# Optimization experiments

Hardware: AMD Instinct MI355X
Metric: run time of the kernel (lower is better)

## Reference

```python
import jax, jax.numpy as jnp
import numpy as np

# ---- static problem configuration (matches init_kwargs) ----
N_PAIRS = 256
NODES_PER_GRAPH = 64
EDGES_PER_GRAPH = 200
MAX_EDGES = 256            # max_edge_set_size
N_GRAPHS = 2 * N_PAIRS     # query/corpus interleaved
N_NODES = N_GRAPHS * NODES_PER_GRAPH
N_EDGES = N_GRAPHS * EDGES_PER_GRAPH
NODE_DIM = 16
EDGE_DIM = 16
H = 128                    # node_state_dim
E_ENC = 64                 # encoded edge feature dim
MSG = 256                  # edge_hidden_sizes[-1] = 2*H (GMN GRU convention)
SK = 32                    # sinkhorn_feature_dim
PROP_STEPS = 5
SK_ITERS = 20
TEMP = 0.1


def setup_inputs() -> dict:
    key = jax.random.key(0)
    ks = jax.random.split(key, 16)
    node_features = jax.random.normal(ks[0], (N_NODES, NODE_DIM), jnp.float32)
    edge_features = jax.random.normal(ks[1], (N_EDGES, EDGE_DIM), jnp.float32)
    # edges are grouped per graph (graph g owns edges [g*E, (g+1)*E)) and
    # endpoints stay inside graph g's node range, as get_graph_features assumes
    offs = np.repeat(np.arange(N_GRAPHS) * NODES_PER_GRAPH, EDGES_PER_GRAPH)
    rng = np.random.default_rng(0)
    from_idx = jnp.asarray(offs + rng.integers(0, NODES_PER_GRAPH, N_EDGES), jnp.int32)
    to_idx = jnp.asarray(offs + rng.integers(0, NODES_PER_GRAPH, N_EDGES), jnp.int32)

    def lin(k, i, o):
        return jax.random.normal(k, (i, o), jnp.float32) / np.sqrt(i).astype(np.float32)

    p = dict(
        enc_node_w=lin(ks[2], NODE_DIM, H), enc_node_b=jnp.zeros((H,), jnp.float32),
        enc_edge_w=lin(ks[3], EDGE_DIM, E_ENC), enc_edge_b=jnp.zeros((E_ENC,), jnp.float32),
        msg_w1=lin(ks[4], 2 * H + E_ENC, MSG), msg_b1=jnp.zeros((MSG,), jnp.float32),
        msg_w2=lin(ks[5], MSG, MSG), msg_b2=jnp.zeros((MSG,), jnp.float32),
        rmsg_w1=lin(ks[6], 2 * H + E_ENC, MSG), rmsg_b1=jnp.zeros((MSG,), jnp.float32),
        rmsg_w2=lin(ks[7], MSG, MSG), rmsg_b2=jnp.zeros((MSG,), jnp.float32),
        gru_w_ih=lin(ks[8], MSG, 3 * H), gru_b_ih=jnp.zeros((3 * H,), jnp.float32),
        gru_w_hh=lin(ks[9], H, 3 * H), gru_b_hh=jnp.zeros((3 * H,), jnp.float32),
        sk_w1=lin(ks[10], MSG, SK), sk_b1=jnp.zeros((SK,), jnp.float32),
        sk_w2=lin(ks[11], SK, SK), sk_b2=jnp.zeros((SK,), jnp.float32),
    )
    return {"node_features": node_features, "edge_features": edge_features,
            "from_idx": from_idx, "to_idx": to_idx, **p}


def _mlp2(x, w1, b1, w2, b2):
    # Linear -> ReLU -> Linear (GMN MLP: no activation after last layer)
    return jax.nn.relu(x @ w1 + b1) @ w2 + b2


def reference(node_features, edge_features, from_idx, to_idx,
              enc_node_w, enc_node_b, enc_edge_w, enc_edge_b,
              msg_w1, msg_b1, msg_w2, msg_b2,
              rmsg_w1, rmsg_b1, rmsg_w2, rmsg_b2,
              gru_w_ih, gru_b_ih, gru_w_hh, gru_b_hh,
              sk_w1, sk_b1, sk_w2, sk_b2):
    # ---- GraphEncoder (single-layer MLPs) ----
    h = node_features @ enc_node_w + enc_node_b          # [N_NODES, H]
    e = edge_features @ enc_edge_w + enc_edge_b          # [N_EDGES, E_ENC]

    def edge_msgs(h):
        s, d = h[from_idx], h[to_idx]                    # gathers [N_EDGES, H]
        fwd = _mlp2(jnp.concatenate([s, d, e], axis=1), msg_w1, msg_b1, msg_w2, msg_b2)
        rev = _mlp2(jnp.concatenate([d, s, e], axis=1), rmsg_w1, rmsg_b1, rmsg_w2, rmsg_b2)
        return fwd, rev                                  # [N_EDGES, MSG] each

    # ---- propagation loop: gather -> edge MLP -> scatter -> GRU update ----
    for _ in range(PROP_STEPS):
        fwd, rev = edge_msgs(h)
        agg = (jax.ops.segment_sum(fwd, to_idx, num_segments=N_NODES)
               + jax.ops.segment_sum(rev, from_idx, num_segments=N_NODES))  # [N_NODES, MSG]
        gi = agg @ gru_w_ih + gru_b_ih                   # [N_NODES, 3H]
        gh = h @ gru_w_hh + gru_b_hh
        r = jax.nn.sigmoid(gi[:, :H] + gh[:, :H])
        z = jax.nn.sigmoid(gi[:, H:2 * H] + gh[:, H:2 * H])
        n = jnp.tanh(gi[:, 2 * H:] + r * gh[:, 2 * H:])
        h = (1.0 - z) * n + z * h                        # torch GRU update

    # ---- propagation_messages: per-edge fwd + rev message ----
    fwd, rev = edge_msgs(h)
    e_final = fwd + rev                                  # [N_EDGES, MSG]

    # ---- split_and_stack: per-graph edge sets padded to MAX_EDGES ----
    stacked = jnp.pad(e_final.reshape(N_GRAPHS, EDGES_PER_GRAPH, MSG),
                      ((0, 0), (0, MAX_EDGES - EDGES_PER_GRAPH), (0, 0)))
    q, c = stacked[0::2], stacked[1::2]                  # [B, MAX_EDGES, MSG]

    # ---- sinkhorn feature MLP + size mask ----
    tq = _mlp2(q, sk_w1, sk_b1, sk_w2, sk_b2)            # [B, MAX_EDGES, SK]
    tc = _mlp2(c, sk_w1, sk_b1, sk_w2, sk_b2)
    mask = (jnp.arange(MAX_EDGES) < EDGES_PER_GRAPH).astype(jnp.float32)[None, :, None]
    mq, mc = mask * tq, mask * tc

    # ---- log-domain Sinkhorn ----
    la = jnp.einsum('bif,bjf->bij', mq, mc) / TEMP       # [B, MAX_EDGES, MAX_EDGES]
    for _ in range(SK_ITERS):
        la = la - jax.nn.logsumexp(la, axis=2, keepdims=True)
        la = la - jax.nn.logsumexp(la, axis=1, keepdims=True)
    plan = jnp.exp(la)

    # ---- feature_alignment_score: -sum relu(q - P @ c) ----
    return -jnp.sum(jax.nn.relu(q - jnp.einsum('bij,bjf->bif', plan, c)), axis=(1, 2))
```

## Files before the change

### kernel.cpp

```cpp
#include <hip/hip_runtime.h>
#include <math.h>

typedef __attribute__((ext_vector_type(4))) float f32x4;
typedef __attribute__((ext_vector_type(8))) short s16x8;
typedef __attribute__((ext_vector_type(4))) short s16x4;

#define NN 32768
#define NE 102400
#define HD 128
#define EED 64
#define MSGD 256
#define NG 512
#define EPG 200
#define NP 256
#define SKD 32

__device__ inline short f2bf(float x){
  union{float f; unsigned u;} z; z.f=x;
  unsigned r = (z.u + 0x7fffu + ((z.u>>16)&1u)) >> 16;
  return (short)r;
}
__device__ inline float bf2f(unsigned short u){
  union{unsigned u; float f;} z; z.u = ((unsigned)u)<<16; return z.f;
}
__device__ inline float frcp(float x){
  float r; asm("v_rcp_f32 %0, %1" : "=v"(r) : "v"(x)); return r;
}

__global__ void __launch_bounds__(256) k_enc_node(const float* __restrict__ nf,
    const float* __restrict__ W, const float* __restrict__ b, float* __restrict__ h){
  __shared__ float Ws[16*128];
  int t = threadIdx.x;
  for (int i=t;i<16*128;i+=256) Ws[i]=W[i];
  __syncthreads();
  int node = blockIdx.x*2 + (t>>7);
  int f = t & 127;
  const float* x = nf + node*16;
  float acc = b[f];
  #pragma unroll
  for (int k=0;k<16;k++) acc = fmaf(x[k], Ws[k*128+f], acc);
  h[node*HD+f] = acc;
}

__global__ void __launch_bounds__(256) k_enc_edge(const float* __restrict__ ef,
    const float* __restrict__ W, const float* __restrict__ b, float* __restrict__ ee){
  __shared__ float Ws[16*64];
  int t = threadIdx.x;
  for (int i=t;i<16*64;i+=256) Ws[i]=W[i];
  __syncthreads();
  int edge = blockIdx.x*4 + (t>>6);
  int f = t & 63;
  const float* x = ef + edge*16;
  float acc = b[f];
  #pragma unroll
  for (int k=0;k<16;k++) acc = fmaf(x[k], Ws[k*64+f], acc);
  ee[edge*EED+f] = acc;
}

__global__ void __launch_bounds__(256) k_pack(const float* __restrict__ W,
    short* __restrict__ dst, int K, int N){
  int NT = N >> 4;
  int i = blockIdx.x*256 + threadIdx.x;
  if (i >= (K/32)*NT*64) return;
  int l = i & 63, tile = i >> 6;
  int nt = tile % NT, kt = tile / NT;
  int lr = l & 15, lq = l >> 4;
  s16x8 v;
  #pragma unroll
  for (int j=0;j<8;j++)
    v[j] = f2bf(W[(size_t)(kt*32 + lq*8 + j)*N + nt*16 + lr]);
  *((s16x8*)dst + i) = v;
}

__global__ void __launch_bounds__(256) k_csr_count(const int* __restrict__ fidx,
    const int* __restrict__ tidx, int* __restrict__ cur_in, int* __restrict__ cur_out){
  int e = blockIdx.x*256 + threadIdx.x;
  if (e >= NE) return;
  atomicAdd(&cur_in[tidx[e]], 1);
  atomicAdd(&cur_out[fidx[e]], 1);
}
__global__ void k_csr_scan(int* __restrict__ cur_in, int* __restrict__ start_in,
    int* __restrict__ cur_out, int* __restrict__ start_out){
  if (threadIdx.x) return;
  int g = blockIdx.x;
  int n0 = g*64, base = g*EPG;
  int run = base;
  for (int i=0;i<64;i++){ int c=cur_in[n0+i]; start_in[n0+i]=run; cur_in[n0+i]=run; run+=c; }
  run = base;
  for (int i=0;i<64;i++){ int c=cur_out[n0+i]; start_out[n0+i]=run; cur_out[n0+i]=run; run+=c; }
}
__global__ void __launch_bounds__(256) k_csr_fill(const int* __restrict__ fidx,
    const int* __restrict__ tidx, int* __restrict__ cur_in, int* __restrict__ cur_out,
    int* __restrict__ list_in, int* __restrict__ list_out){
  int e = blockIdx.x*256 + threadIdx.x;
  if (e >= NE) return;
  int p1 = atomicAdd(&cur_in[tidx[e]], 1);  list_in[p1] = e;
  int p2 = atomicAdd(&cur_out[fidx[e]], 1); list_out[p2] = e;
}

__global__ void __launch_bounds__(256,2) k_msg_both(const float* __restrict__ h,
    const float* __restrict__ ee, const int* __restrict__ from_idx, const int* __restrict__ to_idx,
    const short* __restrict__ w1f, const float* __restrict__ b1f,
    const short* __restrict__ w2f, const float* __restrict__ b2f,
    const short* __restrict__ w1r, const float* __restrict__ b1r,
    const short* __restrict__ w2r, const float* __restrict__ b2r,
    short* __restrict__ mf, short* __restrict__ mr){
  __shared__ __align__(16) short Xs[64][328];
  __shared__ __align__(16) short Ys[64][264];
  __shared__ int sidx[64], didx[64];
  int t = threadIdx.x;
  int e0 = blockIdx.x*64;
  if (t < 64){ sidx[t]=from_idx[e0+t]; didx[t]=to_idx[e0+t]; }
  __syncthreads();
  for (int i=t; i<64*40; i+=256){
    int r = i/40, c8 = (i - r*40)*8;
    const float* src; int off;
    if (c8 < 128){ src = h + (size_t)sidx[r]*HD; off = c8; }
    else if (c8 < 256){ src = h + (size_t)didx[r]*HD; off = c8-128; }
    else { src = ee + (size_t)(e0+r)*EED; off = c8-256; }
    float4 a = *(const float4*)(src+off);
    float4 b = *(const float4*)(src+off+4);
    s16x8 v;
    v[0]=f2bf(a.x); v[1]=f2bf(a.y); v[2]=f2bf(a.z); v[3]=f2bf(a.w);
    v[4]=f2bf(b.x); v[5]=f2bf(b.y); v[6]=f2bf(b.z); v[7]=f2bf(b.w);
    *(s16x8*)&Xs[r][c8] = v;
  }
  __syncthreads();

  int wv = t>>6, l = t&63, lr = l&15, lq = l>>4;
  int cbase = wv*64;

  for (int dir=0; dir<2; dir++){
    const s16x8* W1v = (const s16x8*)(dir ? w1r : w1f);
    const float* B1  = dir ? b1r : b1f;
    const s16x8* W2v = (const s16x8*)(dir ? w2r : w2f);
    const float* B2  = dir ? b2r : b2f;

    f32x4 acc[4][4];
    #pragma unroll
    for (int ct=0; ct<4; ct++){
      float bb = B1[cbase + ct*16 + lr];
      #pragma unroll
      for (int rt=0; rt<4; rt++) acc[rt][ct] = (f32x4){bb,bb,bb,bb};
    }
    {
      s16x8 a0[4], b0[4], b1[4];
      int sc0 = dir ? 4 : 0;
      #pragma unroll
      for (int rt=0;rt<4;rt++) a0[rt] = *(const s16x8*)&Xs[rt*16+lr][sc0*32 + lq*8];
      #pragma unroll
      for (int ct=0;ct<4;ct++) b0[ct] = W1v[(size_t)(0*16 + wv*4 + ct)*64 + l];
      #pragma unroll
      for (int ct=0;ct<4;ct++) b1[ct] = W1v[(size_t)(1*16 + wv*4 + ct)*64 + l];
      #pragma unroll
      for (int kt=0; kt<10; kt++){
        s16x8 an[4], bn[4];
        if (kt < 9){
          int sc = (dir && (kt+1)<8) ? ((kt+1)^4) : (kt+1);
          #pragma unroll
          for (int rt=0;rt<4;rt++) an[rt] = *(const s16x8*)&Xs[rt*16+lr][sc*32 + lq*8];
        }
        if (kt < 8){
          #pragma unroll
          for (int ct=0;ct<4;ct++) bn[ct] = W1v[(size_t)((kt+2)*16 + wv*4 + ct)*64 + l];
        }
        #pragma unroll
        for (int rt=0; rt<4; rt++)
          #pragma unroll
          for (int ct=0; ct<4; ct++)
            acc[rt][ct] = __builtin_amdgcn_mfma_f32_16x16x32_bf16(a0[rt], b0[ct], acc[rt][ct], 0,0,0);
        #pragma unroll
        for (int i=0;i<4;i++){ a0[i]=an[i]; b0[i]=b1[i]; b1[i]=bn[i]; }
      }
    }
    #pragma unroll
    for (int rt=0; rt<4; rt++)
      #pragma unroll
      for (int ct=0; ct<4; ct++)
        #pragma unroll
        for (int r=0; r<4; r++)
          Ys[rt*16 + lq*4 + r][cbase + ct*16 + lr] = f2bf(fmaxf(acc[rt][ct][r], 0.f));
    __syncthreads();

    f32x4 acc2[4][4];
    #pragma unroll
    for (int ct=0; ct<4; ct++){
      float bb = B2[cbase + ct*16 + lr];
      #pragma unroll
      for (int rt=0; rt<4; rt++) acc2[rt][ct] = (f32x4){bb,bb,bb,bb};
    }
    {
      s16x8 a0[4], b0[4], b1[4];
      #pragma unroll
      for (int rt=0;rt<4;rt++) a0[rt] = *(const s16x8*)&Ys[rt*16+lr][lq*8];
      #pragma unroll
      for (int ct=0;ct<4;ct++) b0[ct] = W2v[(size_t)(0*16 + wv*4 + ct)*64 + l];
      #pragma unroll
      for (int ct=0;ct<4;ct++) b1[ct] = W2v[(size_t)(1*16 + wv*4 + ct)*64 + l];
      #pragma unroll
      for (int kt=0; kt<8; kt++){
        s16x8 an[4], bn[4];
        if (kt < 7){
          #pragma unroll
          for (int rt=0;rt<4;rt++) an[rt] = *(const s16x8*)&Ys[rt*16+lr][(kt+1)*32 + lq*8];
        }
        if (kt < 6){
          #pragma unroll
          for (int ct=0;ct<4;ct++) bn[ct] = W2v[(size_t)((kt+2)*16 + wv*4 + ct)*64 + l];
        }
        #pragma unroll
        for (int rt=0; rt<4; rt++)
          #pragma unroll
          for (int ct=0; ct<4; ct++)
            acc2[rt][ct] = __builtin_amdgcn_mfma_f32_16x16x32_bf16(a0[rt], b0[ct], acc2[rt][ct], 0,0,0);
        #pragma unroll
        for (int i=0;i<4;i++){ a0[i]=an[i]; b0[i]=b1[i]; b1[i]=bn[i]; }
      }
    }
    __syncthreads();
    #pragma unroll
    for (int rt=0; rt<4; rt++)
      #pragma unroll
      for (int ct=0; ct<4; ct++)
        #pragma unroll
        for (int r=0; r<4; r++)
          Ys[rt*16 + lq*4 + r][cbase + ct*16 + lr] = f2bf(acc2[rt][ct][r]);
    __syncthreads();
    {
      short* dst = (dir ? mr : mf) + (size_t)e0*MSGD;
      for (int i=t; i<64*32; i+=256){
        int row = i>>5, c8 = (i&31)*8;
        *(s16x8*)&dst[(size_t)row*MSGD + c8] = *(const s16x8*)&Ys[row][c8];
      }
    }
    __syncthreads();
  }
}

__global__ void __launch_bounds__(256) k_gather(const unsigned short* __restrict__ mf,
    const unsigned short* __restrict__ mr,
    const int* __restrict__ start_in, const int* __restrict__ end_in, const int* __restrict__ list_in,
    const int* __restrict__ start_out, const int* __restrict__ end_out, const int* __restrict__ list_out,
    float* __restrict__ agg){
  int n = blockIdx.x*4 + (threadIdx.x>>6);
  int l = threadIdx.x & 63;
  float4 acc = {0.f,0.f,0.f,0.f};
  int s0 = start_in[n], e0 = end_in[n];
  for (int i=s0; i<e0; i++){
    int e = list_in[i];
    ushort4 v = *(const ushort4*)&mf[(size_t)e*MSGD + 4*l];
    acc.x += bf2f(v.x); acc.y += bf2f(v.y); acc.z += bf2f(v.z); acc.w += bf2f(v.w);
  }
  int s1 = start_out[n], e1 = end_out[n];
  for (int i=s1; i<e1; i++){
    int e = list_out[i];
    ushort4 v = *(const ushort4*)&mr[(size_t)e*MSGD + 4*l];
    acc.x += bf2f(v.x); acc.y += bf2f(v.y); acc.z += bf2f(v.z); acc.w += bf2f(v.w);
  }
  *(float4*)&agg[(size_t)n*MSGD + 4*l] = acc;
}

__global__ void __launch_bounds__(256,2) k_msg_fin(const float* __restrict__ h,
    const float* __restrict__ ee, const int* __restrict__ from_idx, const int* __restrict__ to_idx,
    const short* __restrict__ w1f, const float* __restrict__ b1f,
    const short* __restrict__ w2f, const float* __restrict__ b2f,
    const short* __restrict__ w1r, const float* __restrict__ b1r,
    const short* __restrict__ w2r, const float* __restrict__ b2r,
    float* __restrict__ outp){
  __shared__ __align__(16) short Xs[64][328];
  __shared__ __align__(16) short Ys[64][264];
  __shared__ int sidx[64], didx[64];
  int t = threadIdx.x;
  int e0 = blockIdx.x*64;
  if (t < 64){ sidx[t]=from_idx[e0+t]; didx[t]=to_idx[e0+t]; }
  __syncthreads();
  for (int i=t; i<64*40; i+=256){
    int r = i/40, c8 = (i - r*40)*8;
    const float* src; int off;
    if (c8 < 128){ src = h + (size_t)sidx[r]*HD; off = c8; }
    else if (c8 < 256){ src = h + (size_t)didx[r]*HD; off = c8-128; }
    else { src = ee + (size_t)(e0+r)*EED; off = c8-256; }
    float4 a = *(const float4*)(src+off);
    float4 b = *(const float4*)(src+off+4);
    s16x8 v;
    v[0]=f2bf(a.x); v[1]=f2bf(a.y); v[2]=f2bf(a.z); v[3]=f2bf(a.w);
    v[4]=f2bf(b.x); v[5]=f2bf(b.y); v[6]=f2bf(b.z); v[7]=f2bf(b.w);
    *(s16x8*)&Xs[r][c8] = v;
  }
  __syncthreads();

  int wv = t>>6, l = t&63, lr = l&15, lq = l>>4;
  int cbase = wv*64;
  f32x4 fsv[4][4];

  for (int dir=0; dir<2; dir++){
    const s16x8* W1v = (const s16x8*)(dir ? w1r : w1f);
    const float* B1  = dir ? b1r : b1f;
    const s16x8* W2v = (const s16x8*)(dir ? w2r : w2f);
    const float* B2  = dir ? b2r : b2f;

    f32x4 acc[4][4];
    #pragma unroll
    for (int ct=0; ct<4; ct++){
      float bb = B1[cbase + ct*16 + lr];
      #pragma unroll
      for (int rt=0; rt<4; rt++) acc[rt][ct] = (f32x4){bb,bb,bb,bb};
    }
    {
      s16x8 a0[4], b0[4], b1[4];
      int sc0 = dir ? 4 : 0;
      #pragma unroll
      for (int rt=0;rt<4;rt++) a0[rt] = *(const s16x8*)&Xs[rt*16+lr][sc0*32 + lq*8];
      #pragma unroll
      for (int ct=0;ct<4;ct++) b0[ct] = W1v[(size_t)(0*16 + wv*4 + ct)*64 + l];
      #pragma unroll
      for (int ct=0;ct<4;ct++) b1[ct] = W1v[(size_t)(1*16 + wv*4 + ct)*64 + l];
      #pragma unroll
      for (int kt=0; kt<10; kt++){
        s16x8 an[4], bn[4];
        if (kt < 9){
          int sc = (dir && (kt+1)<8) ? ((kt+1)^4) : (kt+1);
          #pragma unroll
          for (int rt=0;rt<4;rt++) an[rt] = *(const s16x8*)&Xs[rt*16+lr][sc*32 + lq*8];
        }
        if (kt < 8){
          #pragma unroll
          for (int ct=0;ct<4;ct++) bn[ct] = W1v[(size_t)((kt+2)*16 + wv*4 + ct)*64 + l];
        }
        #pragma unroll
        for (int rt=0; rt<4; rt++)
          #pragma unroll
          for (int ct=0; ct<4; ct++)
            acc[rt][ct] = __builtin_amdgcn_mfma_f32_16x16x32_bf16(a0[rt], b0[ct], acc[rt][ct], 0,0,0);
        #pragma unroll
        for (int i=0;i<4;i++){ a0[i]=an[i]; b0[i]=b1[i]; b1[i]=bn[i]; }
      }
    }
    #pragma unroll
    for (int rt=0; rt<4; rt++)
      #pragma unroll
      for (int ct=0; ct<4; ct++)
        #pragma unroll
        for (int r=0; r<4; r++)
          Ys[rt*16 + lq*4 + r][cbase + ct*16 + lr] = f2bf(fmaxf(acc[rt][ct][r], 0.f));
    __syncthreads();

    f32x4 acc2[4][4];
    #pragma unroll
    for (int ct=0; ct<4; ct++){
      float bb = B2[cbase + ct*16 + lr];
      #pragma unroll
      for (int rt=0; rt<4; rt++) acc2[rt][ct] = (f32x4){bb,bb,bb,bb};
    }
    {
      s16x8 a0[4], b0[4], b1[4];
      #pragma unroll
      for (int rt=0;rt<4;rt++) a0[rt] = *(const s16x8*)&Ys[rt*16+lr][lq*8];
      #pragma unroll
      for (int ct=0;ct<4;ct++) b0[ct] = W2v[(size_t)(0*16 + wv*4 + ct)*64 + l];
      #pragma unroll
      for (int ct=0;ct<4;ct++) b1[ct] = W2v[(size_t)(1*16 + wv*4 + ct)*64 + l];
      #pragma unroll
      for (int kt=0; kt<8; kt++){
        s16x8 an[4], bn[4];
        if (kt < 7){
          #pragma unroll
          for (int rt=0;rt<4;rt++) an[rt] = *(const s16x8*)&Ys[rt*16+lr][(kt+1)*32 + lq*8];
        }
        if (kt < 6){
          #pragma unroll
          for (int ct=0;ct<4;ct++) bn[ct] = W2v[(size_t)((kt+2)*16 + wv*4 + ct)*64 + l];
        }
        #pragma unroll
        for (int rt=0; rt<4; rt++)
          #pragma unroll
          for (int ct=0; ct<4; ct++)
            acc2[rt][ct] = __builtin_amdgcn_mfma_f32_16x16x32_bf16(a0[rt], b0[ct], acc2[rt][ct], 0,0,0);
        #pragma unroll
        for (int i=0;i<4;i++){ a0[i]=an[i]; b0[i]=b1[i]; b1[i]=bn[i]; }
      }
    }

    if (dir==0){
      #pragma unroll
      for (int rt=0; rt<4; rt++)
        #pragma unroll
        for (int ct=0; ct<4; ct++) fsv[rt][ct] = acc2[rt][ct];
    } else {
      #pragma unroll
      for (int rt=0; rt<4; rt++)
        #pragma unroll
        for (int ct=0; ct<4; ct++)
          #pragma unroll
          for (int r=0; r<4; r++){
            int row = e0 + rt*16 + lq*4 + r;
            outp[(size_t)row*MSGD + cbase + ct*16 + lr] = fsv[rt][ct][r] + acc2[rt][ct][r];
          }
    }
    __syncthreads();
  }
}

__global__ void __launch_bounds__(256,2) k_gru(const float* __restrict__ h,
    const float* __restrict__ agg,
    const short* __restrict__ wih_p, const float* __restrict__ bih,
    const short* __restrict__ whh_p, const float* __restrict__ bhh,
    float* __restrict__ hnew){
  __shared__ __align__(16) short aggs[64][264];
  __shared__ __align__(16) short hs[64][136];
  int t = threadIdx.x;
  int n0 = blockIdx.x*64;
  for (int i=t; i<64*32; i+=256){
    int r = i>>5, c8 = (i&31)*8;
    float4 a = *(const float4*)&agg[(size_t)(n0+r)*MSGD + c8];
    float4 b = *(const float4*)&agg[(size_t)(n0+r)*MSGD + c8 + 4];
    s16x8 v;
    v[0]=f2bf(a.x); v[1]=f2bf(a.y); v[2]=f2bf(a.z); v[3]=f2bf(a.w);
    v[4]=f2bf(b.x); v[5]=f2bf(b.y); v[6]=f2bf(b.z); v[7]=f2bf(b.w);
    *(s16x8*)&aggs[r][c8] = v;
  }
  for (int i=t; i<64*16; i+=256){
    int r = i>>4, c8 = (i&15)*8;
    float4 a = *(const float4*)&h[(size_t)(n0+r)*HD + c8];
    float4 b = *(const float4*)&h[(size_t)(n0+r)*HD + c8 + 4];
    s16x8 v;
    v[0]=f2bf(a.x); v[1]=f2bf(a.y); v[2]=f2bf(a.z); v[3]=f2bf(a.w);
    v[4]=f2bf(b.x); v[5]=f2bf(b.y); v[6]=f2bf(b.z); v[7]=f2bf(b.w);
    *(s16x8*)&hs[r][c8] = v;
  }
  __syncthreads();

  int wv = t>>6, l = t&63, lr = l&15, lq = l>>4;
  const s16x8* Wih_v = (const s16x8*)wih_p;
  const s16x8* Whh_v = (const s16x8*)whh_p;

  f32x4 gi[4][6], gh[4][6];
  #pragma unroll
  for (int ct=0; ct<6; ct++){
    int bcol = (ct>>1)*128 + wv*32 + (ct&1)*16 + lr;
    float bi = bih[bcol], bh = bhh[bcol];
    #pragma unroll
    for (int rt=0; rt<4; rt++){
      gi[rt][ct] = (f32x4){bi,bi,bi,bi};
      gh[rt][ct] = (f32x4){bh,bh,bh,bh};
    }
  }
  for (int kt=0; kt<8; kt++){
    s16x8 af[4], bfr[6];
    #pragma unroll
    for (int rt=0; rt<4; rt++) af[rt] = *(const s16x8*)&aggs[rt*16+lr][kt*32 + lq*8];
    #pragma unroll
    for (int ct=0; ct<6; ct++){
      int nt = (ct>>1)*8 + wv*2 + (ct&1);
      bfr[ct] = Wih_v[(size_t)(kt*24 + nt)*64 + l];
    }
    #pragma unroll
    for (int rt=0; rt<4; rt++)
      #pragma unroll
      for (int ct=0; ct<6; ct++)
        gi[rt][ct] = __builtin_amdgcn_mfma_f32_16x16x32_bf16(af[rt], bfr[ct], gi[rt][ct], 0,0,0);
  }
  for (int kt=0; kt<4; kt++){
    s16x8 af[4], bfr[6];
    #pragma unroll
    for (int rt=0; rt<4; rt++) af[rt] = *(const s16x8*)&hs[rt*16+lr][kt*32 + lq*8];
    #pragma unroll
    for (int ct=0; ct<6; ct++){
      int nt = (ct>>1)*8 + wv*2 + (ct&1);
      bfr[ct] = Whh_v[(size_t)(kt*24 + nt)*64 + l];
    }
    #pragma unroll
    for (int rt=0; rt<4; rt++)
      #pragma unroll
      for (int ct=0; ct<6; ct++)
        gh[rt][ct] = __builtin_amdgcn_mfma_f32_16x16x32_bf16(af[rt], bfr[ct], gh[rt][ct], 0,0,0);
  }
  #pragma unroll
  for (int rt=0; rt<4; rt++)
    #pragma unroll
    for (int j=0; j<2; j++)
      #pragma unroll
      for (int r=0; r<4; r++){
        int row = n0 + rt*16 + lq*4 + r;
        int col = wv*32 + j*16 + lr;
        float rr = 1.f/(1.f + __expf(-(gi[rt][j][r]   + gh[rt][j][r])));
        float zz = 1.f/(1.f + __expf(-(gi[rt][2+j][r] + gh[rt][2+j][r])));
        float gn = gi[rt][4+j][r] + rr*gh[rt][4+j][r];
        float nn = 1.f - 2.f/(__expf(2.f*gn) + 1.f);
        float hold = h[(size_t)row*HD + col];
        hnew[(size_t)row*HD + col] = (1.f - zz)*nn + zz*hold;
      }
}

__global__ void __launch_bounds__(256,2) k_tall(const float* __restrict__ ef,
    const short* __restrict__ W1p, const float* __restrict__ b1,
    const short* __restrict__ W2p, const float* __restrict__ b2,
    float* __restrict__ tall){
  __shared__ __align__(16) short Xs[64][264];
  __shared__ __align__(16) short Ys[64][40];
  int t = threadIdx.x;
  int g = blockIdx.x>>2, r0 = (blockIdx.x&3)*64;
  for (int i=t; i<64*32; i+=256){
    int r = i>>5, c8 = (i&31)*8;
    s16x8 v;
    int row = r0 + r;
    if (row < EPG){
      const float* src = ef + ((size_t)g*EPG + row)*MSGD + c8;
      float4 a = *(const float4*)src;
      float4 b = *(const float4*)(src+4);
      v[0]=f2bf(a.x); v[1]=f2bf(a.y); v[2]=f2bf(a.z); v[3]=f2bf(a.w);
      v[4]=f2bf(b.x); v[5]=f2bf(b.y); v[6]=f2bf(b.z); v[7]=f2bf(b.w);
    } else v = (s16x8){0,0,0,0,0,0,0,0};
    *(s16x8*)&Xs[r][c8] = v;
  }
  __syncthreads();
  int wv = t>>6, l = t&63, lr = l&15, lq = l>>4;
  const s16x8* W1v = (const s16x8*)W1p;
  const s16x8* W2v = (const s16x8*)W2p;
  f32x4 acc[2];
  #pragma unroll
  for (int ct=0; ct<2; ct++){
    float bb = b1[ct*16 + lr];
    acc[ct] = (f32x4){bb,bb,bb,bb};
  }
  for (int kt=0; kt<8; kt++){
    s16x8 a = *(const s16x8*)&Xs[wv*16+lr][kt*32 + lq*8];
    #pragma unroll
    for (int ct=0; ct<2; ct++){
      s16x8 bfr = W1v[(size_t)(kt*2 + ct)*64 + l];
      acc[ct] = __builtin_amdgcn_mfma_f32_16x16x32_bf16(a, bfr, acc[ct], 0,0,0);
    }
  }
  #pragma unroll
  for (int ct=0; ct<2; ct++)
    #pragma unroll
    for (int r=0; r<4; r++)
      Ys[wv*16 + lq*4 + r][ct*16 + lr] = f2bf(fmaxf(acc[ct][r], 0.f));
  __syncthreads();
  f32x4 acc2[2];
  #pragma unroll
  for (int ct=0; ct<2; ct++){
    float bb = b2[ct*16 + lr];
    acc2[ct] = (f32x4){bb,bb,bb,bb};
  }
  {
    s16x8 a = *(const s16x8*)&Ys[wv*16+lr][lq*8];
    #pragma unroll
    for (int ct=0; ct<2; ct++){
      s16x8 bfr = W2v[(size_t)ct*64 + l];
      acc2[ct] = __builtin_amdgcn_mfma_f32_16x16x32_bf16(a, bfr, acc2[ct], 0,0,0);
    }
  }
  #pragma unroll
  for (int ct=0; ct<2; ct++)
    #pragma unroll
    for (int r=0; r<4; r++){
      int row = r0 + wv*16 + lq*4 + r;
      tall[((size_t)g*256 + row)*SKD + ct*16 + lr] = (row < EPG) ? acc2[ct][r] : 0.f;
    }
}

__global__ void __attribute__((amdgpu_waves_per_eu(4,4))) __launch_bounds__(1024)
k_sinkhorn(const float* __restrict__ tall, short* __restrict__ plan){
  __shared__ float tqs[256*32];
  __shared__ float tcsT[32*257];
  __shared__ float cv[256];
  __shared__ float psm[16][256];
  int p = blockIdx.x, t = threadIdx.x;
  int w = t>>6, l = t&63;
  int rbase = w*16;
  const float* tq = tall + (size_t)(2*p)*8192;
  const float* tc = tall + (size_t)(2*p+1)*8192;
  for (int i=t; i<8192; i+=1024){
    tqs[i] = tq[i];
    tcsT[(i&31)*257 + (i>>5)] = tc[i];
  }
  __syncthreads();
  float4 E[16];
  #pragma unroll
  for (int k=0; k<16; k++){
    float4 a = {0.f,0.f,0.f,0.f};
    for (int kk=0; kk<32; kk+=4){
      float4 c0 = *(const float4*)&tcsT[(kk+0)*257 + 4*l];
      float4 c1 = *(const float4*)&tcsT[(kk+1)*257 + 4*l];
      float4 c2 = *(const float4*)&tcsT[(kk+2)*257 + 4*l];
      float4 c3 = *(const float4*)&tcsT[(kk+3)*257 + 4*l];
      float4 q = *(const float4*)&tqs[(rbase+k)*32 + kk];
      a.x = fmaf(q.x,c0.x, fmaf(q.y,c1.x, fmaf(q.z,c2.x, fmaf(q.w,c3.x, a.x))));
      a.y = fmaf(q.x,c0.y, fmaf(q.y,c1.y, fmaf(q.z,c2.y, fmaf(q.w,c3.y, a.y))));
      a.z = fmaf(q.x,c0.z, fmaf(q.y,c1.z, fmaf(q.z,c2.z, fmaf(q.w,c3.z, a.z))));
      a.w = fmaf(q.x,c0.w, fmaf(q.y,c1.w, fmaf(q.z,c2.w, fmaf(q.w,c3.w, a.w))));
    }
    a.x *= 10.f; a.y *= 10.f; a.z *= 10.f; a.w *= 10.f;
    float m = fmaxf(fmaxf(a.x,a.y), fmaxf(a.z,a.w));
    #pragma unroll
    for (int off=32; off; off>>=1) m = fmaxf(m, __shfl_xor(m, off));
    float s = __expf(a.x-m)+__expf(a.y-m)+__expf(a.z-m)+__expf(a.w-m);
    #pragma unroll
    for (int off=32; off; off>>=1) s += __shfl_xor(s, off);
    float r = m + __logf(s);
    E[k].x = __expf(a.x - r); E[k].y = __expf(a.y - r);
    E[k].z = __expf(a.z - r); E[k].w = __expf(a.w - r);
  }

  for (int it=0; it<20; it++){
    float4 sm = {0.f,0.f,0.f,0.f};
    #pragma unroll
    for (int k=0;k<16;k++){
      sm.x += E[k].x; sm.y += E[k].y; sm.z += E[k].z; sm.w += E[k].w;
    }
    *(float4*)&psm[w][4*l] = sm;
    __syncthreads();
    if (t < 256){
      float s = psm[0][t];
      #pragma unroll
      for (int ww=1; ww<16; ww++) s += psm[ww][t];
      cv[t] = frcp(s);
    }
    __syncthreads();
    float4 ic = *(const float4*)&cv[4*l];
    #pragma unroll
    for (int k=0;k<16;k++){
      E[k].x *= ic.x; E[k].y *= ic.y; E[k].z *= ic.z; E[k].w *= ic.w;
    }
    if (it < 19){
      #pragma unroll
      for (int k=0;k<16;k++){
        float s = E[k].x + E[k].y + E[k].z + E[k].w;
        #pragma unroll
        for (int off=32; off; off>>=1) s += __shfl_xor(s, off);
        float inv = frcp(s);
        E[k].x *= inv; E[k].y *= inv; E[k].z *= inv; E[k].w *= inv;
      }
    }
  }
  short* P = plan + (size_t)p*65536;
  #pragma unroll
  for (int k=0;k<16;k++){
    s16x4 o;
    o[0]=f2bf(E[k].x); o[1]=f2bf(E[k].y); o[2]=f2bf(E[k].z); o[3]=f2bf(E[k].w);
    *(s16x4*)&P[(size_t)(rbase+k)*256 + 4*l] = o;
  }
}

__global__ void __launch_bounds__(256,2) k_loss(const short* __restrict__ plan,
    const float* __restrict__ ef, float* __restrict__ out){
  __shared__ __align__(16) short Ps[128][40];
  __shared__ __align__(16) short Cs[256][40];
  __shared__ float red[4];
  int t = threadIdx.x;
  int b = blockIdx.x, p = b>>1, rh = b&1;
  int i0 = rh*128;
  int wv = t>>6, l = t&63, lr = l&15, lq = l>>4;
  const short* Pb = plan + (size_t)p*65536;
  const float* C = ef + (size_t)(2*p+1)*EPG*MSGD;
  const float* Q = ef + (size_t)(2*p)*EPG*MSGD;

  f32x4 acc[2][16];
  #pragma unroll
  for (int rt=0;rt<2;rt++)
    #pragma unroll
    for (int ct=0;ct<16;ct++) acc[rt][ct] = (f32x4){0.f,0.f,0.f,0.f};

  for (int kt=0; kt<8; kt++){
    __syncthreads();
    for (int i=t; i<128*4; i+=256){
      int r = i>>2, c8 = (i&3)*8;
      *(s16x8*)&Ps[r][c8] = *(const s16x8*)&Pb[(size_t)(i0+r)*256 + kt*32 + c8];
    }
    for (int i=t; i<32*64; i+=256){
      int k = i>>6, c4 = (i&63)*4;
      int j = kt*32 + k;
      float4 v = (j < EPG) ? *(const float4*)&C[(size_t)j*256 + c4] : (float4){0.f,0.f,0.f,0.f};
      Cs[c4+0][k]=f2bf(v.x); Cs[c4+1][k]=f2bf(v.y); Cs[c4+2][k]=f2bf(v.z); Cs[c4+3][k]=f2bf(v.w);
    }
    __syncthreads();
    s16x8 a0 = *(const s16x8*)&Ps[wv*32      + lr][lq*8];
    s16x8 a1 = *(const s16x8*)&Ps[wv*32 + 16 + lr][lq*8];
    #pragma unroll
    for (int ct=0; ct<16; ct++){
      s16x8 bfr = *(const s16x8*)&Cs[ct*16+lr][lq*8];
      acc[0][ct] = __builtin_amdgcn_mfma_f32_16x16x32_bf16(a0, bfr, acc[0][ct], 0,0,0);
      acc[1][ct] = __builtin_amdgcn_mfma_f32_16x16x32_bf16(a1, bfr, acc[1][ct], 0,0,0);
    }
  }
  float s = 0.f;
  #pragma unroll
  for (int rt=0; rt<2; rt++)
    #pragma unroll
    for (int ct=0; ct<16; ct++)
      #pragma unroll
      for (int r=0; r<4; r++){
        int row = i0 + wv*32 + rt*16 + lq*4 + r;
        int col = ct*16 + lr;
        float q = (row < EPG) ? Q[(size_t)row*256 + col] : 0.f;
        s += fmaxf(q - acc[rt][ct][r], 0.f);
      }
  #pragma unroll
  for (int off=32; off; off>>=1) s += __shfl_xor(s, off);
  if (l==0) red[wv] = s;
  __syncthreads();
  if (t==0) atomicAdd(&out[p], -(red[0]+red[1]+red[2]+red[3]));
}

extern "C" void kernel_launch(void* const* d_in, const int* in_sizes, int n_in,
                              void* d_out, int out_size, void* d_ws, size_t ws_size,
                              hipStream_t stream){
  const float* nf   = (const float*)d_in[0];
  const float* ef   = (const float*)d_in[1];
  const int*   fidx = (const int*)d_in[2];
  const int*   tidx = (const int*)d_in[3];
  const float* enw  = (const float*)d_in[4];
  const float* enb  = (const float*)d_in[5];
  const float* eew  = (const float*)d_in[6];
  const float* eeb  = (const float*)d_in[7];
  const float* mw1  = (const float*)d_in[8];
  const float* mb1  = (const float*)d_in[9];
  const float* mw2  = (const float*)d_in[10];
  const float* mb2  = (const float*)d_in[11];
  const float* rw1  = (const float*)d_in[12];
  const float* rb1  = (const float*)d_in[13];
  const float* rw2  = (const float*)d_in[14];
  const float* rb2  = (const float*)d_in[15];
  const float* wih  = (const float*)d_in[16];
  const float* bih  = (const float*)d_in[17];
  const float* whh  = (const float*)d_in[18];
  const float* bhh  = (const float*)d_in[19];
  const float* skw1 = (const float*)d_in[20];
  const float* skb1 = (const float*)d_in[21];
  const float* skw2 = (const float*)d_in[22];
  const float* skb2 = (const float*)d_in[23];
  float* out = (float*)d_out;

  float* ws = (float*)d_ws;
  float* h_a    = ws;
  float* h_b    = h_a + (size_t)NN*HD;
  float* e_enc  = h_b + (size_t)NN*HD;
  float* e_fin  = e_enc + (size_t)NE*EED;
  float* t_all  = e_fin + (size_t)NE*MSGD;
  float* la     = t_all + (size_t)NG*256*SKD;

  short* mf = (short*)e_fin;
  short* mr = mf + (size_t)NE*MSGD;

  short* w1f_p = (short*)t_all;
  short* w1r_p = w1f_p + 320*256;
  short* w2f_p = w1r_p + 320*256;
  short* w2r_p = w2f_p + 256*256;
  short* wih_p = w2r_p + 256*256;
  short* whh_p = wih_p + 256*384;
  int*   csr   = (int*)(t_all + 221184);
  int* cur_in    = csr;
  int* cur_out   = cur_in  + NN;
  int* start_in  = cur_out + NN;
  int* start_out = start_in + NN;
  int* list_in   = start_out + NN;
  int* list_out  = list_in + NE;

  float* agg    = la;
  short* plan_s = (short*)la;
  short* skw1_p = (short*)(la + 9000000);
  short* skw2_p = skw1_p + 256*32;

  k_pack<<<40, 256, 0, stream>>>(mw1, w1f_p, 320, 256);
  k_pack<<<40, 256, 0, stream>>>(rw1, w1r_p, 320, 256);
  k_pack<<<32, 256, 0, stream>>>(mw2, w2f_p, 256, 256);
  k_pack<<<32, 256, 0, stream>>>(rw2, w2r_p, 256, 256);
  k_pack<<<48, 256, 0, stream>>>(wih, wih_p, 256, 384);
  k_pack<<<24, 256, 0, stream>>>(whh, whh_p, 128, 384);
  k_pack<<<4, 256, 0, stream>>>(skw1, skw1_p, 256, 32);
  k_pack<<<1, 256, 0, stream>>>(skw2, skw2_p, 32, 32);

  k_enc_node<<<NN/2, 256, 0, stream>>>(nf, enw, enb, h_a);
  k_enc_edge<<<NE/4, 256, 0, stream>>>(ef, eew, eeb, e_enc);

  hipMemsetAsync(csr, 0, (size_t)2*NN*sizeof(int), stream);
  k_csr_count<<<NE/256, 256, 0, stream>>>(fidx, tidx, cur_in, cur_out);
  k_csr_scan<<<NG, 64, 0, stream>>>(cur_in, start_in, cur_out, start_out);
  k_csr_fill<<<NE/256, 256, 0, stream>>>(fidx, tidx, cur_in, cur_out, list_in, list_out);

  float* hc = h_a; float* hn = h_b;
  for (int step=0; step<5; step++){
    k_msg_both<<<NE/64, 256, 0, stream>>>(hc, e_enc, fidx, tidx,
        w1f_p, mb1, w2f_p, mb2, w1r_p, rb1, w2r_p, rb2, mf, mr);
    k_gather<<<NN/4, 256, 0, stream>>>((const unsigned short*)mf, (const unsigned short*)mr,
        start_in, cur_in, list_in, start_out, cur_out, list_out, agg);
    k_gru<<<NN/64, 256, 0, stream>>>(hc, agg, wih_p, bih, whh_p, bhh, hn);
    float* tmp = hc; hc = hn; hn = tmp;
  }
  k_msg_fin<<<NE/64, 256, 0, stream>>>(hc, e_enc, fidx, tidx,
      w1f_p, mb1, w2f_p, mb2, w1r_p, rb1, w2r_p, rb2, e_fin);

  k_tall<<<NG*4, 256, 0, stream>>>(e_fin, skw1_p, skb1, skw2_p, skb2, t_all);
  k_sinkhorn<<<NP, 1024, 0, stream>>>(t_all, plan_s);

  hipMemsetAsync(out, 0, (size_t)NP*sizeof(float), stream);
  k_loss<<<NP*2, 256, 0, stream>>>(plan_s, e_fin, out);
}
```

Baseline: 1.118 ms.

## Store intermediate activations in bf16 to halve gather and load traffic

Node states, encoded edges, aggregated messages and final edge messages are now written in bf16 alongside (or instead of) fp32, so downstream kernels load bf16 directly instead of reading fp32 and converting. This cuts global memory traffic in the message, GRU, tall and loss kernels and removes repeated conversions. The cost is extra bf16 writes for h and an earlier loss of precision: agg and e_final are rounded to bf16 before the GRU and the loss use them. The q term in the loss now also reads bf16.

```diff
diff --git a/kernel.cpp b/kernel.cpp
--- a/kernel.cpp
+++ b/kernel.cpp
@@ -28,7 +28,8 @@
 }
 
 __global__ void __launch_bounds__(256) k_enc_node(const float* __restrict__ nf,
-    const float* __restrict__ W, const float* __restrict__ b, float* __restrict__ h){
+    const float* __restrict__ W, const float* __restrict__ b,
+    float* __restrict__ h, short* __restrict__ hb){
   __shared__ float Ws[16*128];
   int t = threadIdx.x;
   for (int i=t;i<16*128;i+=256) Ws[i]=W[i];
@@ -40,10 +41,11 @@
   #pragma unroll
   for (int k=0;k<16;k++) acc = fmaf(x[k], Ws[k*128+f], acc);
   h[node*HD+f] = acc;
+  hb[node*HD+f] = f2bf(acc);
 }
 
 __global__ void __launch_bounds__(256) k_enc_edge(const float* __restrict__ ef,
-    const float* __restrict__ W, const float* __restrict__ b, float* __restrict__ ee){
+    const float* __restrict__ W, const float* __restrict__ b, short* __restrict__ eeb){
   __shared__ float Ws[16*64];
   int t = threadIdx.x;
   for (int i=t;i<16*64;i+=256) Ws[i]=W[i];
@@ -54,7 +56,7 @@
   float acc = b[f];
   #pragma unroll
   for (int k=0;k<16;k++) acc = fmaf(x[k], Ws[k*64+f], acc);
-  ee[edge*EED+f] = acc;
+  eeb[edge*EED+f] = f2bf(acc);
 }
 
 __global__ void __launch_bounds__(256) k_pack(const float* __restrict__ W,
@@ -98,8 +100,8 @@
   int p2 = atomicAdd(&cur_out[fidx[e]], 1); list_out[p2] = e;
 }
 
-__global__ void __launch_bounds__(256,2) k_msg_both(const float* __restrict__ h,
-    const float* __restrict__ ee, const int* __restrict__ from_idx, const int* __restrict__ to_idx,
+__global__ void __launch_bounds__(256,2) k_msg_both(const short* __restrict__ hb,
+    const short* __restrict__ eeb, const int* __restrict__ from_idx, const int* __restrict__ to_idx,
     const short* __restrict__ w1f, const float* __restrict__ b1f,
     const short* __restrict__ w2f, const float* __restrict__ b2f,
     const short* __restrict__ w1r, const float* __restrict__ b1r,
@@ -114,16 +116,11 @@
   __syncthreads();
   for (int i=t; i<64*40; i+=256){
     int r = i/40, c8 = (i - r*40)*8;
-    const float* src; int off;
-    if (c8 < 128){ src = h + (size_t)sidx[r]*HD; off = c8; }
-    else if (c8 < 256){ src = h + (size_t)didx[r]*HD; off = c8-128; }
-    else { src = ee + (size_t)(e0+r)*EED; off = c8-256; }
-    float4 a = *(const float4*)(src+off);
-    float4 b = *(const float4*)(src+off+4);
-    s16x8 v;
-    v[0]=f2bf(a.x); v[1]=f2bf(a.y); v[2]=f2bf(a.z); v[3]=f2bf(a.w);
-    v[4]=f2bf(b.x); v[5]=f2bf(b.y); v[6]=f2bf(b.z); v[7]=f2bf(b.w);
-    *(s16x8*)&Xs[r][c8] = v;
+    const short* src;
+    if (c8 < 128)      src = hb + (size_t)sidx[r]*HD + c8;
+    else if (c8 < 256) src = hb + (size_t)didx[r]*HD + (c8-128);
+    else               src = eeb + (size_t)(e0+r)*EED + (c8-256);
+    *(s16x8*)&Xs[r][c8] = *(const s16x8*)src;
   }
   __syncthreads();
 
@@ -241,7 +238,7 @@
     const unsigned short* __restrict__ mr,
     const int* __restrict__ start_in, const int* __restrict__ end_in, const int* __restrict__ list_in,
     const int* __restrict__ start_out, const int* __restrict__ end_out, const int* __restrict__ list_out,
-    float* __restrict__ agg){
+    short* __restrict__ aggb){
   int n = blockIdx.x*4 + (threadIdx.x>>6);
   int l = threadIdx.x & 63;
   float4 acc = {0.f,0.f,0.f,0.f};
@@ -257,16 +254,18 @@
     ushort4 v = *(const ushort4*)&mr[(size_t)e*MSGD + 4*l];
     acc.x += bf2f(v.x); acc.y += bf2f(v.y); acc.z += bf2f(v.z); acc.w += bf2f(v.w);
   }
-  *(float4*)&agg[(size_t)n*MSGD + 4*l] = acc;
-}
-
-__global__ void __launch_bounds__(256,2) k_msg_fin(const float* __restrict__ h,
-    const float* __restrict__ ee, const int* __restrict__ from_idx, const int* __restrict__ to_idx,
+  s16x4 o;
+  o[0]=f2bf(acc.x); o[1]=f2bf(acc.y); o[2]=f2bf(acc.z); o[3]=f2bf(acc.w);
+  *(s16x4*)&aggb[(size_t)n*MSGD + 4*l] = o;
+}
+
+__global__ void __launch_bounds__(256,2) k_msg_fin(const short* __restrict__ hb,
+    const short* __restrict__ eeb, const int* __restrict__ from_idx, const int* __restrict__ to_idx,
     const short* __restrict__ w1f, const float* __restrict__ b1f,
     const short* __restrict__ w2f, const float* __restrict__ b2f,
     const short* __restrict__ w1r, const float* __restrict__ b1r,
     const short* __restrict__ w2r, const float* __restrict__ b2r,
-    float* __restrict__ outp){
+    short* __restrict__ efb){
   __shared__ __align__(16) short Xs[64][328];
   __shared__ __align__(16) short Ys[64][264];
   __shared__ int sidx[64], didx[64];
@@ -276,16 +275,11 @@
   __syncthreads();
   for (int i=t; i<64*40; i+=256){
     int r = i/40, c8 = (i - r*40)*8;
-    const float* src; int off;
-    if (c8 < 128){ src = h + (size_t)sidx[r]*HD; off = c8; }
-    else if (c8 < 256){ src = h + (size_t)didx[r]*HD; off = c8-128; }
-    else { src = ee + (size_t)(e0+r)*EED; off = c8-256; }
-    float4 a = *(const float4*)(src+off);
-    float4 b = *(const float4*)(src+off+4);
-    s16x8 v;
-    v[0]=f2bf(a.x); v[1]=f2bf(a.y); v[2]=f2bf(a.z); v[3]=f2bf(a.w);
-    v[4]=f2bf(b.x); v[5]=f2bf(b.y); v[6]=f2bf(b.z); v[7]=f2bf(b.w);
-    *(s16x8*)&Xs[r][c8] = v;
+    const short* src;
+    if (c8 < 128)      src = hb + (size_t)sidx[r]*HD + c8;
+    else if (c8 < 256) src = hb + (size_t)didx[r]*HD + (c8-128);
+    else               src = eeb + (size_t)(e0+r)*EED + (c8-256);
+    *(s16x8*)&Xs[r][c8] = *(const s16x8*)src;
   }
   __syncthreads();
 
@@ -386,47 +380,42 @@
       for (int rt=0; rt<4; rt++)
         #pragma unroll
         for (int ct=0; ct<4; ct++) fsv[rt][ct] = acc2[rt][ct];
+      __syncthreads();
     } else {
+      __syncthreads();
       #pragma unroll
       for (int rt=0; rt<4; rt++)
         #pragma unroll
         for (int ct=0; ct<4; ct++)
           #pragma unroll
-          for (int r=0; r<4; r++){
-            int row = e0 + rt*16 + lq*4 + r;
-            outp[(size_t)row*MSGD + cbase + ct*16 + lr] = fsv[rt][ct][r] + acc2[rt][ct][r];
-          }
-    }
-    __syncthreads();
+          for (int r=0; r<4; r++)
+            Ys[rt*16 + lq*4 + r][cbase + ct*16 + lr] = f2bf(fsv[rt][ct][r] + acc2[rt][ct][r]);
+      __syncthreads();
+      short* dst = efb + (size_t)e0*MSGD;
+      for (int i=t; i<64*32; i+=256){
+        int row = i>>5, c8 = (i&31)*8;
+        *(s16x8*)&dst[(size_t)row*MSGD + c8] = *(const s16x8*)&Ys[row][c8];
+      }
+    }
   }
 }
 
 __global__ void __launch_bounds__(256,2) k_gru(const float* __restrict__ h,
-    const float* __restrict__ agg,
+    const short* __restrict__ hb, const short* __restrict__ aggb,
     const short* __restrict__ wih_p, const float* __restrict__ bih,
     const short* __restrict__ whh_p, const float* __restrict__ bhh,
-    float* __restrict__ hnew){
+    float* __restrict__ hnew, short* __restrict__ hnewb){
   __shared__ __align__(16) short aggs[64][264];
   __shared__ __align__(16) short hs[64][136];
   int t = threadIdx.x;
   int n0 = blockIdx.x*64;
   for (int i=t; i<64*32; i+=256){
     int r = i>>5, c8 = (i&31)*8;
-    float4 a = *(const float4*)&agg[(size_t)(n0+r)*MSGD + c8];
-    float4 b = *(const float4*)&agg[(size_t)(n0+r)*MSGD + c8 + 4];
-    s16x8 v;
-    v[0]=f2bf(a.x); v[1]=f2bf(a.y); v[2]=f2bf(a.z); v[3]=f2bf(a.w);
-    v[4]=f2bf(b.x); v[5]=f2bf(b.y); v[6]=f2bf(b.z); v[7]=f2bf(b.w);
-    *(s16x8*)&aggs[r][c8] = v;
+    *(s16x8*)&aggs[r][c8] = *(const s16x8*)&aggb[(size_t)(n0+r)*MSGD + c8];
   }
   for (int i=t; i<64*16; i+=256){
     int r = i>>4, c8 = (i&15)*8;
-    float4 a = *(const float4*)&h[(size_t)(n0+r)*HD + c8];
-    float4 b = *(const float4*)&h[(size_t)(n0+r)*HD + c8 + 4];
-    s16x8 v;
-    v[0]=f2bf(a.x); v[1]=f2bf(a.y); v[2]=f2bf(a.z); v[3]=f2bf(a.w);
-    v[4]=f2bf(b.x); v[5]=f2bf(b.y); v[6]=f2bf(b.z); v[7]=f2bf(b.w);
-    *(s16x8*)&hs[r][c8] = v;
+    *(s16x8*)&hs[r][c8] = *(const s16x8*)&hb[(size_t)(n0+r)*HD + c8];
   }
   __syncthreads();
 
@@ -488,11 +477,13 @@
         float gn = gi[rt][4+j][r] + rr*gh[rt][4+j][r];
         float nn = 1.f - 2.f/(__expf(2.f*gn) + 1.f);
         float hold = h[(size_t)row*HD + col];
-        hnew[(size_t)row*HD + col] = (1.f - zz)*nn + zz*hold;
-      }
-}
-
-__global__ void __launch_bounds__(256,2) k_tall(const float* __restrict__ ef,
+        float hv = (1.f - zz)*nn + zz*hold;
+        hnew[(size_t)row*HD + col] = hv;
+        hnewb[(size_t)row*HD + col] = f2bf(hv);
+      }
+}
+
+__global__ void __launch_bounds__(256,2) k_tall(const short* __restrict__ efb,
     const short* __restrict__ W1p, const float* __restrict__ b1,
     const short* __restrict__ W2p, const float* __restrict__ b2,
     float* __restrict__ tall){
@@ -502,15 +493,9 @@
   int g = blockIdx.x>>2, r0 = (blockIdx.x&3)*64;
   for (int i=t; i<64*32; i+=256){
     int r = i>>5, c8 = (i&31)*8;
-    s16x8 v;
     int row = r0 + r;
-    if (row < EPG){
-      const float* src = ef + ((size_t)g*EPG + row)*MSGD + c8;
-      float4 a = *(const float4*)src;
-      float4 b = *(const float4*)(src+4);
-      v[0]=f2bf(a.x); v[1]=f2bf(a.y); v[2]=f2bf(a.z); v[3]=f2bf(a.w);
-      v[4]=f2bf(b.x); v[5]=f2bf(b.y); v[6]=f2bf(b.z); v[7]=f2bf(b.w);
-    } else v = (s16x8){0,0,0,0,0,0,0,0};
+    s16x8 v = (row < EPG) ? *(const s16x8*)&efb[((size_t)g*EPG + row)*MSGD + c8]
+                          : (s16x8){0,0,0,0,0,0,0,0};
     *(s16x8*)&Xs[r][c8] = v;
   }
   __syncthreads();
@@ -644,7 +629,7 @@
 }
 
 __global__ void __launch_bounds__(256,2) k_loss(const short* __restrict__ plan,
-    const float* __restrict__ ef, float* __restrict__ out){
+    const short* __restrict__ efb, float* __restrict__ out){
   __shared__ __align__(16) short Ps[128][40];
   __shared__ __align__(16) short Cs[256][40];
   __shared__ float red[4];
@@ -653,8 +638,8 @@
   int i0 = rh*128;
   int wv = t>>6, l = t&63, lr = l&15, lq = l>>4;
   const short* Pb = plan + (size_t)p*65536;
-  const float* C = ef + (size_t)(2*p+1)*EPG*MSGD;
-  const float* Q = ef + (size_t)(2*p)*EPG*MSGD;
+  const unsigned short* C = (const unsigned short*)(efb + (size_t)(2*p+1)*EPG*MSGD);
+  const unsigned short* Q = (const unsigned short*)(efb + (size_t)(2*p)*EPG*MSGD);
 
   f32x4 acc[2][16];
   #pragma unroll
@@ -671,8 +656,8 @@
     for (int i=t; i<32*64; i+=256){
       int k = i>>6, c4 = (i&63)*4;
       int j = kt*32 + k;
-      float4 v = (j < EPG) ? *(const float4*)&C[(size_t)j*256 + c4] : (float4){0.f,0.f,0.f,0.f};
-      Cs[c4+0][k]=f2bf(v.x); Cs[c4+1][k]=f2bf(v.y); Cs[c4+2][k]=f2bf(v.z); Cs[c4+3][k]=f2bf(v.w);
+      ushort4 v = (j < EPG) ? *(const ushort4*)&C[(size_t)j*256 + c4] : (ushort4){0,0,0,0};
+      Cs[c4+0][k]=(short)v.x; Cs[c4+1][k]=(short)v.y; Cs[c4+2][k]=(short)v.z; Cs[c4+3][k]=(short)v.w;
     }
     __syncthreads();
     s16x8 a0 = *(const s16x8*)&Ps[wv*32      + lr][lq*8];
@@ -693,7 +678,7 @@
       for (int r=0; r<4; r++){
         int row = i0 + wv*32 + rt*16 + lq*4 + r;
         int col = ct*16 + lr;
-        float q = (row < EPG) ? Q[(size_t)row*256 + col] : 0.f;
+        float q = (row < EPG) ? bf2f(Q[(size_t)row*256 + col]) : 0.f;
         s += fmaxf(q - acc[rt][ct][r], 0.f);
       }
   #pragma unroll
@@ -713,7 +698,7 @@
   const float* enw  = (const float*)d_in[4];
   const float* enb  = (const float*)d_in[5];
   const float* eew  = (const float*)d_in[6];
-  const float* eeb  = (const float*)d_in[7];
+  const float* eeb_w= (const float*)d_in[7];
   const float* mw1  = (const float*)d_in[8];
   const float* mb1  = (const float*)d_in[9];
   const float* mw2  = (const float*)d_in[10];
@@ -733,15 +718,16 @@
   float* out = (float*)d_out;
 
   float* ws = (float*)d_ws;
-  float* h_a    = ws;
-  float* h_b    = h_a + (size_t)NN*HD;
-  float* e_enc  = h_b + (size_t)NN*HD;
-  float* e_fin  = e_enc + (size_t)NE*EED;
-  float* t_all  = e_fin + (size_t)NE*MSGD;
-  float* la     = t_all + (size_t)NG*256*SKD;
-
-  short* mf = (short*)e_fin;
-  short* mr = mf + (size_t)NE*MSGD;
+  float* h_a   = ws;
+  float* h_b   = h_a + (size_t)NN*HD;
+  short* hb_a  = (short*)(h_b + (size_t)NN*HD);
+  short* hb_b  = hb_a + (size_t)NN*HD;
+  short* ee_b  = hb_b + (size_t)NN*HD;
+  short* mf    = ee_b + (size_t)NE*EED;
+  short* mr    = mf + (size_t)NE*MSGD;
+  short* e_finb = mf;
+  float* t_all = (float*)(mr + (size_t)NE*MSGD);
+  float* la    = t_all + (size_t)NG*256*SKD;
 
   short* w1f_p = (short*)t_all;
   short* w1r_p = w1f_p + 320*256;
@@ -757,7 +743,7 @@
   int* list_in   = start_out + NN;
   int* list_out  = list_in + NE;
 
-  float* agg    = la;
+  short* aggb   = (short*)la;
   short* plan_s = (short*)la;
   short* skw1_p = (short*)(la + 9000000);
   short* skw2_p = skw1_p + 256*32;
@@ -771,8 +757,8 @@
   k_pack<<<4, 256, 0, stream>>>(skw1, skw1_p, 256, 32);
   k_pack<<<1, 256, 0, stream>>>(skw2, skw2_p, 32, 32);
 
-  k_enc_node<<<NN/2, 256, 0, stream>>>(nf, enw, enb, h_a);
-  k_enc_edge<<<NE/4, 256, 0, stream>>>(ef, eew, eeb, e_enc);
+  k_enc_node<<<NN/2, 256, 0, stream>>>(nf, enw, enb, h_a, hb_a);
+  k_enc_edge<<<NE/4, 256, 0, stream>>>(ef, eew, eeb_w, ee_b);
 
   hipMemsetAsync(csr, 0, (size_t)2*NN*sizeof(int), stream);
   k_csr_count<<<NE/256, 256, 0, stream>>>(fidx, tidx, cur_in, cur_out);
@@ -780,20 +766,22 @@
   k_csr_fill<<<NE/256, 256, 0, stream>>>(fidx, tidx, cur_in, cur_out, list_in, list_out);
 
   float* hc = h_a; float* hn = h_b;
+  short* hbc = hb_a; short* hbn = hb_b;
   for (int step=0; step<5; step++){
-    k_msg_both<<<NE/64, 256, 0, stream>>>(hc, e_enc, fidx, tidx,
+    k_msg_both<<<NE/64, 256, 0, stream>>>(hbc, ee_b, fidx, tidx,
         w1f_p, mb1, w2f_p, mb2, w1r_p, rb1, w2r_p, rb2, mf, mr);
     k_gather<<<NN/4, 256, 0, stream>>>((const unsigned short*)mf, (const unsigned short*)mr,
-        start_in, cur_in, list_in, start_out, cur_out, list_out, agg);
-    k_gru<<<NN/64, 256, 0, stream>>>(hc, agg, wih_p, bih, whh_p, bhh, hn);
+        start_in, cur_in, list_in, start_out, cur_out, list_out, aggb);
+    k_gru<<<NN/64, 256, 0, stream>>>(hc, hbc, aggb, wih_p, bih, whh_p, bhh, hn, hbn);
     float* tmp = hc; hc = hn; hn = tmp;
-  }
-  k_msg_fin<<<NE/64, 256, 0, stream>>>(hc, e_enc, fidx, tidx,
-      w1f_p, mb1, w2f_p, mb2, w1r_p, rb1, w2r_p, rb2, e_fin);
-
-  k_tall<<<NG*4, 256, 0, stream>>>(e_fin, skw1_p, skb1, skw2_p, skb2, t_all);
+    short* tmb = hbc; hbc = hbn; hbn = tmb;
+  }
+  k_msg_fin<<<NE/64, 256, 0, stream>>>(hbc, ee_b, fidx, tidx,
+      w1f_p, mb1, w2f_p, mb2, w1r_p, rb1, w2r_p, rb2, e_finb);
+
+  k_tall<<<NG*4, 256, 0, stream>>>(e_finb, skw1_p, skb1, skw2_p, skb2, t_all);
   k_sinkhorn<<<NP, 1024, 0, stream>>>(t_all, plan_s);
 
   hipMemsetAsync(out, 0, (size_t)NP*sizeof(float), stream);
-  k_loss<<<NP*2, 256, 0, stream>>>(plan_s, e_fin, out);
-}
+  k_loss<<<NP*2, 256, 0, stream>>>(plan_s, e_finb, out);
+}
```

Result: faster. 1.085 ms (-2.9%).
